# Kernel optimization log

Measured on AMD Instinct MI355X. Metric: run time of the kernel, lower is better.

## Reference

```python
import jax, jax.numpy as jnp
import numpy as np

B, L, H, O, C = 64, 32, 128, 16384, 32


def setup_inputs() -> dict:
    key = jax.random.key(0)
    ks = jax.random.split(key, 8)
    s = lambda k, shp, fan: jax.random.normal(k, shp, jnp.float32) / np.sqrt(fan)
    return {
        "z": jax.random.normal(ks[0], (B, L), jnp.float32),
        "feature_embedding": jax.random.normal(ks[1], (O, C), jnp.float32),
        "feature_bias": jax.random.normal(ks[2], (O, 1), jnp.float32),
        "Wz": s(ks[3], (L, H), L),
        "bz": jnp.zeros((H,), jnp.float32),
        "W1": s(ks[4], (H + C + 1, H), H + C + 1),
        "b1": jnp.zeros((H,), jnp.float32),
        "W2": s(ks[5], (H, 1), H),
        "b2": jnp.zeros((1,), jnp.float32),
    }


def reference(z, feature_embedding, feature_bias, Wz, bz, W1, b1, W2, b2):
    # z_processor: Linear + ReLU (dropout_rate=0)
    pz = jax.nn.relu(z @ Wz + bz)  # [B, H]
    # concat([pz, F, b], -1) @ W1  ==  pz@W1_h + F@W1_f + b*W1_b  (no [B,O,H+C+1] materialization)
    W1_h, W1_f, W1_b = W1[:H], W1[H:H + C], W1[H + C:]  # [H,H],[C,H],[1,H]
    h = jax.nn.relu(
        (pz @ W1_h)[:, None, :]                    # [B,1,H]
        + (feature_embedding @ W1_f)[None, :, :]   # [1,O,H]
        + feature_bias * W1_b                      # [O,H] broadcast
        + b1
    )  # [B, O, H]
    out = jnp.einsum("boh,ho->bo", h, W2) + b2  # [B, O]
    return out
```

## Files before the change

kernel.cpp:

```cpp
#include <hip/hip_runtime.h>

#define Bb 64
#define Ll 32
#define Hh 128
#define Oo 16384
#define Cc 32
#define TOo 64
#define NT 512


__global__ __launch_bounds__(256) void prep_kernel(
    const float* __restrict__ z, const float* __restrict__ Wz,
    const float* __restrict__ bz, const float* __restrict__ W1,
    const float* __restrict__ b1, const float* __restrict__ W2,
    const float* __restrict__ b2,
    float* __restrict__ A, float* __restrict__ SA2w,
    float* __restrict__ w2h, float* __restrict__ w1t,
    float* __restrict__ gcoef)
{
    __shared__ float pz[2][Hh];
    __shared__ float ps[2][Hh];
    const int t  = threadIdx.x;
    const int h  = t & (Hh - 1);
    const int bb = t >> 7;
    const int b  = blockIdx.x * 2 + bb;

    float v = bz[h];
#pragma unroll
    for (int c = 0; c < Ll; ++c)
        v = fmaf(z[b * Ll + c], Wz[c * Hh + h], v);
    pz[bb][h] = fmaxf(v, 0.f);
    __syncthreads();

    float a = 0.f;
#pragma unroll
    for (int k = 0; k < Hh; ++k)
        a = fmaf(pz[bb][k], W1[k * Hh + h], a);
    A[b * Hh + h] = a;
    ps[bb][h] = 0.5f * W2[h] * a;
    __syncthreads();

    if (h == 0) {
        float s = b2[0];
        for (int k = 0; k < Hh; ++k) s += ps[bb][k];
        SA2w[b] = s;
    }

    if (t < 128) {
        const int h2 = blockIdx.x * 4 + (t >> 5);
        const int c  = t & 31;
        w1t[h2 * Cc + c] = W1[(Hh + c) * Hh + h2];
    }
    if (t < 4) {
        const int h2 = blockIdx.x * 4 + t;
        w2h[h2] = 0.5f * W2[h2];
        gcoef[2 * h2 + 0] = W1[(Hh + Cc) * Hh + h2];
        gcoef[2 * h2 + 1] = b1[h2];
    }
}

__global__ __launch_bounds__(NT) void main_kernel(
    const float* __restrict__ A,   const float* __restrict__ SA2w,
    const float* __restrict__ fe,  const float* __restrict__ fb,
    const float* __restrict__ w2h, const float* __restrict__ w1t,
    const float* __restrict__ gcoef, float* __restrict__ out)
{
    __shared__ __align__(16) float fe_s[TOo][36];
    __shared__ float g_s[Hh][TOo + 1];

    const int t    = threadIdx.x;
    const int o0   = blockIdx.x * TOo;
    const int lane = t & 63;
    const int wave = __builtin_amdgcn_readfirstlane(t >> 6);

    {
        const float4 f4 = ((const float4*)(fe + o0 * Cc))[t];
        *(float4*)&fe_s[t >> 3][(t & 7) << 2] = f4;
    }
    __syncthreads();

    float4 fer[8];
#pragma unroll
    for (int k = 0; k < 8; ++k)
        fer[k] = *(const float4*)&fe_s[lane][4 * k];
    const float fbv = fb[o0 + lane];

    const int h0 = wave * 16;
#pragma unroll 1
    for (int j = 0; j < 16; ++j) {
        const int h = h0 + j;
        const float w1b = gcoef[2 * h + 0];
        const float b1h = gcoef[2 * h + 1];
        const float* __restrict__ wt = w1t + h * Cc;
        float g = fmaf(fbv, w1b, b1h);
#pragma unroll
        for (int k = 0; k < 8; ++k) {
            g = fmaf(fer[k].x, wt[4 * k + 0], g);
            g = fmaf(fer[k].y, wt[4 * k + 1], g);
            g = fmaf(fer[k].z, wt[4 * k + 2], g);
            g = fmaf(fer[k].w, wt[4 * k + 3], g);
        }
        g_s[h][lane] = g;
    }
    __syncthreads();

    const int b0 = wave * 8;
    float acc[8];
#pragma unroll
    for (int bi = 0; bi < 8; ++bi) acc[bi] = 0.f;
    float sg = 0.f;

#pragma unroll 1
    for (int tt = 0; tt < 8; ++tt) {
        float gj[16];
#pragma unroll
        for (int jr = 0; jr < 16; ++jr)
            gj[jr] = g_s[16 * tt + jr][lane];
        const float* __restrict__ wp = w2h + 16 * tt;
        float w[16];
#pragma unroll
        for (int jr = 0; jr < 16; ++jr) w[jr] = wp[jr];
#pragma unroll
        for (int jr = 0; jr < 16; ++jr)
            sg = fmaf(w[jr], gj[jr], sg);
#pragma unroll
        for (int bi = 0; bi < 8; ++bi) {
            const float* __restrict__ Ap = A + (b0 + bi) * Hh + 16 * tt;
#pragma unroll
            for (int jr = 0; jr < 16; ++jr)
                acc[bi] = fmaf(__builtin_fabsf(gj[jr] + Ap[jr]), w[jr], acc[bi]);
        }
    }

#pragma unroll
    for (int bi = 0; bi < 8; ++bi) {
        const int b = b0 + bi;
        out[b * Oo + o0 + lane] = acc[bi] + sg + SA2w[b];
    }
}

extern "C" void kernel_launch(void* const* d_in, const int* in_sizes, int n_in,
                              void* d_out, int out_size, void* d_ws, size_t ws_size,
                              hipStream_t stream) {
    (void)in_sizes; (void)n_in; (void)out_size; (void)ws_size;
    const float* z   = (const float*)d_in[0];
    const float* fe  = (const float*)d_in[1];
    const float* fb  = (const float*)d_in[2];
    const float* Wz  = (const float*)d_in[3];
    const float* bz  = (const float*)d_in[4];
    const float* W1  = (const float*)d_in[5];
    const float* b1  = (const float*)d_in[6];
    const float* W2  = (const float*)d_in[7];
    const float* b2  = (const float*)d_in[8];
    float* out   = (float*)d_out;
    float* A     = (float*)d_ws;
    float* SA2w  = A + Bb * Hh;
    float* w2h   = SA2w + Bb;
    float* w1t   = w2h + Hh;
    float* gcoef = w1t + Hh * Cc;

    prep_kernel<<<Bb / 2, 256, 0, stream>>>(z, Wz, bz, W1, b1, W2, b2,
                                            A, SA2w, w2h, w1t, gcoef);
    main_kernel<<<Oo / TOo, NT, 0, stream>>>(A, SA2w, fe, fb, w2h, w1t,
                                             gcoef, out);
}
```

Measured before the change: 96.66 us.

## Split fused main kernel into separate G-compute and reduction kernels via global buffer

Replaces the single fused kernel, which computed the feature projection G into shared memory and then reduced over H, with two kernels. The first writes G for all features to a global workspace in an interleaved-pair layout. The second reads it back with more blocks, each covering fewer batch rows. This raises parallelism from 256 blocks to 512 and 1024 blocks and drops shared memory and barriers. The cost is an extra 8 MB round trip through global memory plus an additional kernel launch.

Result: no change. 97.29 us (+0.6%).

```diff
diff --git a/kernel.cpp b/kernel.cpp
--- a/kernel.cpp
+++ b/kernel.cpp
@@ -5,8 +5,6 @@
 #define Hh 128
 #define Oo 16384
 #define Cc 32
-#define TOo 64
-#define NT 512
 
 
 __global__ __launch_bounds__(256) void prep_kernel(
@@ -59,84 +57,92 @@
     }
 }
 
-__global__ __launch_bounds__(NT) void main_kernel(
-    const float* __restrict__ A,   const float* __restrict__ SA2w,
-    const float* __restrict__ fe,  const float* __restrict__ fb,
-    const float* __restrict__ w2h, const float* __restrict__ w1t,
-    const float* __restrict__ gcoef, float* __restrict__ out)
+__global__ __launch_bounds__(256) void g_kernel(
+    const float* __restrict__ fe, const float* __restrict__ fb,
+    const float* __restrict__ w1t, const float* __restrict__ gcoef,
+    float* __restrict__ g_t)
 {
-    __shared__ __align__(16) float fe_s[TOo][36];
-    __shared__ float g_s[Hh][TOo + 1];
-
     const int t    = threadIdx.x;
-    const int o0   = blockIdx.x * TOo;
     const int lane = t & 63;
     const int wave = __builtin_amdgcn_readfirstlane(t >> 6);
-
-    {
-        const float4 f4 = ((const float4*)(fe + o0 * Cc))[t];
-        *(float4*)&fe_s[t >> 3][(t & 7) << 2] = f4;
-    }
-    __syncthreads();
+    const int o    = (blockIdx.x & 255) * 64 + lane;
+    const int hb   = (blockIdx.x >> 8) * 64 + wave * 16;
 
     float4 fer[8];
+    const float4* fep = (const float4*)(fe + o * Cc);
 #pragma unroll
-    for (int k = 0; k < 8; ++k)
-        fer[k] = *(const float4*)&fe_s[lane][4 * k];
-    const float fbv = fb[o0 + lane];
+    for (int k = 0; k < 8; ++k) fer[k] = fep[k];
+    const float fbv = fb[o];
 
-    const int h0 = wave * 16;
 #pragma unroll 1
-    for (int j = 0; j < 16; ++j) {
-        const int h = h0 + j;
-        const float w1b = gcoef[2 * h + 0];
-        const float b1h = gcoef[2 * h + 1];
-        const float* __restrict__ wt = w1t + h * Cc;
-        float g = fmaf(fbv, w1b, b1h);
+    for (int j = 0; j < 8; ++j) {
+        const int h = hb + 2 * j;
+        const float* __restrict__ wt0 = w1t + (h + 0) * Cc;
+        const float* __restrict__ wt1 = w1t + (h + 1) * Cc;
+        float g0 = fmaf(fbv, gcoef[2 * h + 0], gcoef[2 * h + 1]);
+        float g1 = fmaf(fbv, gcoef[2 * h + 2], gcoef[2 * h + 3]);
 #pragma unroll
         for (int k = 0; k < 8; ++k) {
-            g = fmaf(fer[k].x, wt[4 * k + 0], g);
-            g = fmaf(fer[k].y, wt[4 * k + 1], g);
-            g = fmaf(fer[k].z, wt[4 * k + 2], g);
-            g = fmaf(fer[k].w, wt[4 * k + 3], g);
+            g0 = fmaf(fer[k].x, wt0[4 * k + 0], g0);
+            g0 = fmaf(fer[k].y, wt0[4 * k + 1], g0);
+            g0 = fmaf(fer[k].z, wt0[4 * k + 2], g0);
+            g0 = fmaf(fer[k].w, wt0[4 * k + 3], g0);
+            g1 = fmaf(fer[k].x, wt1[4 * k + 0], g1);
+            g1 = fmaf(fer[k].y, wt1[4 * k + 1], g1);
+            g1 = fmaf(fer[k].z, wt1[4 * k + 2], g1);
+            g1 = fmaf(fer[k].w, wt1[4 * k + 3], g1);
         }
-        g_s[h][lane] = g;
+        const int hp = (hb >> 1) + j;
+        *(float2*)(g_t + hp * (2 * Oo) + 2 * o) = make_float2(g0, g1);
     }
-    __syncthreads();
+}
 
-    const int b0 = wave * 8;
-    float acc[8];
-#pragma unroll
-    for (int bi = 0; bi < 8; ++bi) acc[bi] = 0.f;
-    float sg = 0.f;
+__global__ __launch_bounds__(256) void m_kernel(
+    const float* __restrict__ A, const float* __restrict__ SA2w,
+    const float* __restrict__ w2h, const float* __restrict__ g_t,
+    float* __restrict__ out)
+{
+    const int t    = threadIdx.x;
+    const int lane = t & 63;
+    const int wave = __builtin_amdgcn_readfirstlane(t >> 6);
+    const int o    = (blockIdx.x & 255) * 64 + lane;
+    const int b0   = (blockIdx.x >> 8) * 16 + wave * 4;
+
+    const float* __restrict__ A0 = A + (b0 + 0) * Hh;
+    const float* __restrict__ A1 = A + (b0 + 1) * Hh;
+    const float* __restrict__ A2 = A + (b0 + 2) * Hh;
+    const float* __restrict__ A3 = A + (b0 + 3) * Hh;
+
+    float acc0 = 0.f, acc1 = 0.f, acc2 = 0.f, acc3 = 0.f, sg = 0.f;
 
 #pragma unroll 1
-    for (int tt = 0; tt < 8; ++tt) {
-        float gj[16];
+    for (int hc = 0; hc < 16; ++hc) {
+        const int h0 = hc * 8;
+        float g[8];
 #pragma unroll
-        for (int jr = 0; jr < 16; ++jr)
-            gj[jr] = g_s[16 * tt + jr][lane];
-        const float* __restrict__ wp = w2h + 16 * tt;
-        float w[16];
+        for (int k = 0; k < 4; ++k) {
+            const float2 g2 = *(const float2*)(g_t + (4 * hc + k) * (2 * Oo) + 2 * o);
+            g[2 * k + 0] = g2.x;
+            g[2 * k + 1] = g2.y;
+        }
 #pragma unroll
-        for (int jr = 0; jr < 16; ++jr) w[jr] = wp[jr];
-#pragma unroll
-        for (int jr = 0; jr < 16; ++jr)
-            sg = fmaf(w[jr], gj[jr], sg);
-#pragma unroll
-        for (int bi = 0; bi < 8; ++bi) {
-            const float* __restrict__ Ap = A + (b0 + bi) * Hh + 16 * tt;
-#pragma unroll
-            for (int jr = 0; jr < 16; ++jr)
-                acc[bi] = fmaf(__builtin_fabsf(gj[jr] + Ap[jr]), w[jr], acc[bi]);
+        for (int j = 0; j < 8; ++j) {
+            const int h = h0 + j;
+            const float w = w2h[h];
+            sg   = fmaf(w, g[j], sg);
+            acc0 = fmaf(__builtin_fabsf(A0[h] + g[j]), w, acc0);
+            acc1 = fmaf(__builtin_fabsf(A1[h] + g[j]), w, acc1);
+            acc2 = fmaf(__builtin_fabsf(A2[h] + g[j]), w, acc2);
+            acc3 = fmaf(__builtin_fabsf(A3[h] + g[j]), w, acc3);
         }
     }
 
-#pragma unroll
-    for (int bi = 0; bi < 8; ++bi) {
-        const int b = b0 + bi;
-        out[b * Oo + o0 + lane] = acc[bi] + sg + SA2w[b];
-    }
+    const float s0 = SA2w[b0 + 0], s1 = SA2w[b0 + 1];
+    const float s2 = SA2w[b0 + 2], s3 = SA2w[b0 + 3];
+    out[(b0 + 0) * Oo + o] = acc0 + sg + s0;
+    out[(b0 + 1) * Oo + o] = acc1 + sg + s1;
+    out[(b0 + 2) * Oo + o] = acc2 + sg + s2;
+    out[(b0 + 3) * Oo + o] = acc3 + sg + s3;
 }
 
 extern "C" void kernel_launch(void* const* d_in, const int* in_sizes, int n_in,
@@ -158,9 +164,10 @@
     float* w2h   = SA2w + Bb;
     float* w1t   = w2h + Hh;
     float* gcoef = w1t + Hh * Cc;
+    float* g_t   = (float*)d_ws + 16384;
 
     prep_kernel<<<Bb / 2, 256, 0, stream>>>(z, Wz, bz, W1, b1, W2, b2,
                                             A, SA2w, w2h, w1t, gcoef);
-    main_kernel<<<Oo / TOo, NT, 0, stream>>>(A, SA2w, fe, fb, w2h, w1t,
-                                             gcoef, out);
+    g_kernel<<<512, 256, 0, stream>>>(fe, fb, w1t, gcoef, g_t);
+    m_kernel<<<1024, 256, 0, stream>>>(A, SA2w, w2h, g_t, out);
 }
```

## Split main kernel work over H and batch with 1024 threads and LDS reduction

Applied to the files above, without the earlier changes.

Doubles the block to 1024 threads and partitions the work so each wave covers a 32-wide slice of H and 16 batch rows, holding its g and W2 values in registers. The four H-slice partial sums are then reduced through shared memory before the output is written. The embedding tile is now read straight from global memory rather than staged through LDS. This trades lower per-thread register reuse and an extra reduction pass plus more LDS for higher parallelism inside each block.

After: 92.90 us. -3.9%, faster.

```diff
diff --git a/kernel.cpp b/kernel.cpp
--- a/kernel.cpp
+++ b/kernel.cpp
@@ -6,7 +6,7 @@
 #define Oo 16384
 #define Cc 32
 #define TOo 64
-#define NT 512
+#define NT 1024
 
 
 __global__ __launch_bounds__(256) void prep_kernel(
@@ -60,13 +60,13 @@
 }
 
 __global__ __launch_bounds__(NT) void main_kernel(
-    const float* __restrict__ A,   const float* __restrict__ SA2w,
-    const float* __restrict__ fe,  const float* __restrict__ fb,
+    const float* __restrict__ A,  const float* __restrict__ SA2w,
+    const float* __restrict__ fe, const float* __restrict__ fb,
     const float* __restrict__ w2h, const float* __restrict__ w1t,
     const float* __restrict__ gcoef, float* __restrict__ out)
 {
-    __shared__ __align__(16) float fe_s[TOo][36];
-    __shared__ float g_s[Hh][TOo + 1];
+    __shared__ float g_s[Hh][TOo];
+    __shared__ float part[4][Bb][TOo];
 
     const int t    = threadIdx.x;
     const int o0   = blockIdx.x * TOo;
@@ -74,68 +74,72 @@
     const int wave = __builtin_amdgcn_readfirstlane(t >> 6);
 
     {
-        const float4 f4 = ((const float4*)(fe + o0 * Cc))[t];
-        *(float4*)&fe_s[t >> 3][(t & 7) << 2] = f4;
+        float4 fer[8];
+        const float4* fep = (const float4*)(fe + (o0 + lane) * Cc);
+#pragma unroll
+        for (int k = 0; k < 8; ++k) fer[k] = fep[k];
+        const float fbv = fb[o0 + lane];
+        const int hG0 = wave * 8;
+#pragma unroll
+        for (int j = 0; j < 8; ++j) {
+            const int h = hG0 + j;
+            const float* __restrict__ wt = w1t + h * Cc;
+            float g = fmaf(fbv, gcoef[2 * h + 0], gcoef[2 * h + 1]);
+#pragma unroll
+            for (int k = 0; k < 8; ++k) {
+                g = fmaf(fer[k].x, wt[4 * k + 0], g);
+                g = fmaf(fer[k].y, wt[4 * k + 1], g);
+                g = fmaf(fer[k].z, wt[4 * k + 2], g);
+                g = fmaf(fer[k].w, wt[4 * k + 3], g);
+            }
+            g_s[h][lane] = g;
+        }
     }
     __syncthreads();
 
-    float4 fer[8];
+    const int hh = wave & 3, bg = wave >> 2;
+    const int h0 = hh * 32,  b0 = bg * 16;
+
+    float gv[32];
 #pragma unroll
-    for (int k = 0; k < 8; ++k)
-        fer[k] = *(const float4*)&fe_s[lane][4 * k];
-    const float fbv = fb[o0 + lane];
+    for (int k = 0; k < 32; ++k)
+        gv[k] = g_s[h0 + k][lane];
 
-    const int h0 = wave * 16;
-#pragma unroll 1
-    for (int j = 0; j < 16; ++j) {
-        const int h = h0 + j;
-        const float w1b = gcoef[2 * h + 0];
-        const float b1h = gcoef[2 * h + 1];
-        const float* __restrict__ wt = w1t + h * Cc;
-        float g = fmaf(fbv, w1b, b1h);
+    float w2v[32];
 #pragma unroll
-        for (int k = 0; k < 8; ++k) {
-            g = fmaf(fer[k].x, wt[4 * k + 0], g);
-            g = fmaf(fer[k].y, wt[4 * k + 1], g);
-            g = fmaf(fer[k].z, wt[4 * k + 2], g);
-            g = fmaf(fer[k].w, wt[4 * k + 3], g);
-        }
-        g_s[h][lane] = g;
-    }
-    __syncthreads();
+    for (int k = 0; k < 32; ++k)
+        w2v[k] = w2h[h0 + k];
 
-    const int b0 = wave * 8;
-    float acc[8];
+    float sg = 0.f;
 #pragma unroll
-    for (int bi = 0; bi < 8; ++bi) acc[bi] = 0.f;
-    float sg = 0.f;
+    for (int k = 0; k < 32; ++k)
+        sg = fmaf(w2v[k], gv[k], sg);
 
-#pragma unroll 1
-    for (int tt = 0; tt < 8; ++tt) {
-        float gj[16];
+    float acc[16];
 #pragma unroll
-        for (int jr = 0; jr < 16; ++jr)
-            gj[jr] = g_s[16 * tt + jr][lane];
-        const float* __restrict__ wp = w2h + 16 * tt;
-        float w[16];
+    for (int bi = 0; bi < 16; ++bi) acc[bi] = sg;
+
 #pragma unroll
-        for (int jr = 0; jr < 16; ++jr) w[jr] = wp[jr];
+    for (int bi = 0; bi < 16; ++bi) {
+        const float* __restrict__ Ab = A + (b0 + bi) * Hh + h0;
+        float a = acc[bi];
 #pragma unroll
-        for (int jr = 0; jr < 16; ++jr)
-            sg = fmaf(w[jr], gj[jr], sg);
-#pragma unroll
-        for (int bi = 0; bi < 8; ++bi) {
-            const float* __restrict__ Ap = A + (b0 + bi) * Hh + 16 * tt;
-#pragma unroll
-            for (int jr = 0; jr < 16; ++jr)
-                acc[bi] = fmaf(__builtin_fabsf(gj[jr] + Ap[jr]), w[jr], acc[bi]);
-        }
+        for (int k = 0; k < 32; ++k)
+            a = fmaf(__builtin_fabsf(Ab[k] + gv[k]), w2v[k], a);
+        acc[bi] = a;
     }
 
 #pragma unroll
-    for (int bi = 0; bi < 8; ++bi) {
-        const int b = b0 + bi;
-        out[b * Oo + o0 + lane] = acc[bi] + sg + SA2w[b];
+    for (int bi = 0; bi < 16; ++bi)
+        part[hh][b0 + bi][lane] = acc[bi];
+    __syncthreads();
+
+#pragma unroll
+    for (int q = 0; q < 4; ++q) {
+        const int b = wave * 4 + q;
+        const float r = part[0][b][lane] + part[1][b][lane]
+                      + part[2][b][lane] + part[3][b][lane];
+        out[b * Oo + o0 + lane] = r + SA2w[b];
     }
 }
 
```
